# Optimization experiments

Measured on AMD Instinct MI355X. Metric: run time of the kernel, lower is better.

## Reference

```python
import jax, jax.numpy as jnp
import numpy as np

B, S, D, E = 32, 16, 64, 768  # batch, max summary segments, max doc splits, embed dim
EPS = 1e-12


def _l2norm(x):
    # tf.nn.l2_normalize: x * rsqrt(max(sum(x^2), eps))
    return x * jax.lax.rsqrt(jnp.maximum(jnp.sum(x * x, axis=-1, keepdims=True), EPS))


def setup_inputs() -> dict:
    key = jax.random.key(0)
    ks = jax.random.split(key, 12)
    nd = jax.random.randint(ks[0], (B,), 1, D + 1)
    ns = jax.random.randint(ks[1], (B,), 1, S + 1)
    doc = jax.random.normal(ks[2], (B, D, E), jnp.float32)
    seg = jax.random.normal(ks[3], (B, S, E), jnp.float32)
    # emulate RaggedTensor.to_tensor(): zero padding beyond ragged lengths
    doc = doc * (jnp.arange(D)[None, :, None] < nd[:, None, None])
    seg = seg * (jnp.arange(S)[None, :, None] < ns[:, None, None])
    tis = jax.random.uniform(ks[4], (B, S), jnp.float32)
    tis = jnp.where(jnp.arange(S)[None, :] < ns[:, None], tis, 1.0)
    tagg = jax.random.uniform(ks[5], (B,), jnp.float32)
    s1, s2, s3 = 1.0 / np.sqrt(2 * E), 1.0 / np.sqrt(E), 1.0 / np.sqrt(E // 2)
    W1 = jax.random.normal(ks[6], (2 * E, E), jnp.float32) * s1
    W2 = jax.random.normal(ks[7], (E, E // 2), jnp.float32) * s2
    W3 = jax.random.normal(ks[8], (E // 2, 1), jnp.float32) * s3
    return {
        'document_splits_embedding': doc,
        'summary_sentences_embedding': seg,
        'num_document_splits': nd,
        'num_summary_segments': ns,
        'target_agg_score': tagg,
        'target_instance_score': tis,
        'W1': W1, 'b1': jnp.zeros((E,), jnp.float32),
        'W2': W2, 'b2': jnp.zeros((E // 2,), jnp.float32),
        'W3': W3, 'b3': jnp.zeros((1,), jnp.float32),
    }


def reference(document_splits_embedding, summary_sentences_embedding,
              num_document_splits, num_summary_segments,
              target_agg_score, target_instance_score,
              W1, b1, W2, b2, W3, b3):
    doc, seg = document_splits_embedding, summary_sentences_embedding
    nd, ns = num_document_splits, num_summary_segments
    b, d, e = doc.shape
    s = seg.shape[1]
    nsf = ns.astype(jnp.float32)

    # target_instance_score padded with 1.0 beyond ragged length (done in setup; pass through)
    tis = target_instance_score

    # ---- pairwise MLP over all (segment, doc_split) pairs ----
    pair = jnp.concatenate([
        jnp.broadcast_to(doc[:, None, :, :], (b, s, d, e)),
        jnp.broadcast_to(seg[:, :, None, :], (b, s, d, e)),
    ], axis=-1)                                             # [B,S,D,2E]
    h = jax.nn.gelu(pair @ W1 + b1, approximate=False)      # [B,S,D,E]
    h = jax.nn.gelu(h @ W2 + b2, approximate=False)         # [B,S,D,E/2]
    mlp_out = jax.nn.sigmoid(h @ W3 + b3)[..., 0]           # [B,S,D]

    doc_mask = (jnp.arange(d)[None, :] < nd[:, None]).astype(jnp.float32)  # [B,D]
    scored = doc_mask[:, None, :] * mlp_out                # mask invalid doc splits
    pred0 = jnp.max(scored, axis=2)                         # [B,S]
    seg_scale = jnp.where(ns > 10, 1.0, 100.0)[:, None]     # faithful to mask+(1-mask)*100
    pred = seg_scale * pred0                                # [B,S]

    # ---- cosine similarity prior (keras CosineSimilarity = -cos) ----
    dn = _l2norm(doc)                                       # [B,D,E]
    sn = _l2norm(seg)                                       # [B,S,E]
    cos = jnp.einsum('bse,bde->bsd', sn, dn)                # [B,S,D]
    sim = doc_mask[:, None, :] * (1.0 + (-cos)) / 2.0
    doc_cos = jnp.max(sim, axis=2)                          # [B,S]
    seg_mask = (jnp.arange(s)[None, :] < ns[:, None]).astype(jnp.float32)
    diff = jnp.abs(doc_cos - pred) * seg_mask
    cos_prior = jnp.mean(jnp.sum(diff, axis=1) / nsf)

    # ---- correlation prior: Pearson correlation over the 768 'sample' axis ----
    c = seg - jnp.mean(seg, axis=-1, keepdims=True)
    z = c * jax.lax.rsqrt(jnp.maximum(jnp.sum(c * c, axis=-1, keepdims=True), EPS))
    R = (1.0 + jnp.einsum('bse,bte->bst', z, z)) / 2.0      # [B,S,S]
    p = pred
    t1 = (1.0 - p)[:, :, None] * (1.0 - p)[:, None, :]
    t2 = p[:, :, None] * p[:, None, :]
    pair_mask = seg_mask[:, :, None] * seg_mask[:, None, :]
    term = jnp.abs(t1 - R) * jnp.abs(t2 - R) * pair_mask
    corr_prior = jnp.mean(jnp.sum(term, axis=(1, 2)) / nsf)

    return (target_agg_score, tis, pred, ns, cos_prior, corr_prior)
```

## Files before the change

### kernel.cpp

```cpp
#include <hip/hip_runtime.h>
#include <hip/hip_bf16.h>
#include <math.h>

#define EPSF 1e-12f

typedef short bf16x8 __attribute__((ext_vector_type(8)));
typedef float f32x4  __attribute__((ext_vector_type(4)));

__device__ __forceinline__ float gelu_fast(float x) {
    float x2 = x * x;
    float z = -2.3021184f * x * fmaf(0.044715f, x2, 1.0f);
    float u = __builtin_amdgcn_exp2f(z);
    return x * __builtin_amdgcn_rcpf(1.0f + u);
}
__device__ __forceinline__ float sigmoid_fast(float x) {
    float u = __builtin_amdgcn_exp2f(-1.44269504f * x);
    return __builtin_amdgcn_rcpf(1.0f + u);
}
__device__ __forceinline__ float bf2f(unsigned short u) {
    return __uint_as_float(((unsigned int)u) << 16);
}
__device__ __forceinline__ unsigned short f2bf(float f) {
    unsigned int u = __float_as_uint(f);
    u += 0x7FFFu + ((u >> 16) & 1u);
    return (unsigned short)(u >> 16);
}

__global__ __launch_bounds__(256) void k_prep(
    const float* __restrict__ doc, const float* __restrict__ seg,
    const float* __restrict__ W1, const float* __restrict__ W2,
    const float* __restrict__ tagg, const float* __restrict__ tis,
    const int* __restrict__ ns,
    float* __restrict__ dscale, float* __restrict__ sscale,
    float* __restrict__ smean, float* __restrict__ cscale,
    unsigned short* __restrict__ docB, unsigned short* __restrict__ segB,
    unsigned short* __restrict__ W1T, unsigned short* __restrict__ W2T,
    float* __restrict__ out)
{
    __shared__ float sT[64][65];
    int blk = blockIdx.x;
    int t = threadIdx.x;
    if (blk == 1000) {
        if (t < 32) out[t] = tagg[t];
        out[32 + t] = tis[t];
        out[32 + 256 + t] = tis[256 + t];
        if (t < 32) out[1056 + t] = (float)ns[t];
        return;
    }
    if (blk < 640) {
        int row = blk * 4 + (t >> 6);
        int lane = t & 63;
        const float* src = (row < 2048) ? (doc + (size_t)row * 768)
                                        : (seg + (size_t)(row - 2048) * 768);
        unsigned short* dst = (row < 2048) ? (docB + (size_t)row * 768)
                                           : (segB + (size_t)(row - 2048) * 768);
        float ss = 0.f, sm = 0.f;
        float4 v0 = *(const float4*)(src + lane * 4);
        float4 v1 = *(const float4*)(src + lane * 4 + 256);
        float4 v2 = *(const float4*)(src + lane * 4 + 512);
        ss += v0.x * v0.x + v0.y * v0.y + v0.z * v0.z + v0.w * v0.w;
        ss += v1.x * v1.x + v1.y * v1.y + v1.z * v1.z + v1.w * v1.w;
        ss += v2.x * v2.x + v2.y * v2.y + v2.z * v2.z + v2.w * v2.w;
        sm += v0.x + v0.y + v0.z + v0.w;
        sm += v1.x + v1.y + v1.z + v1.w;
        sm += v2.x + v2.y + v2.z + v2.w;
        {
            ushort4 o;
            o.x = f2bf(v0.x); o.y = f2bf(v0.y); o.z = f2bf(v0.z); o.w = f2bf(v0.w);
            *(ushort4*)(dst + lane * 4) = o;
            o.x = f2bf(v1.x); o.y = f2bf(v1.y); o.z = f2bf(v1.z); o.w = f2bf(v1.w);
            *(ushort4*)(dst + lane * 4 + 256) = o;
            o.x = f2bf(v2.x); o.y = f2bf(v2.y); o.z = f2bf(v2.z); o.w = f2bf(v2.w);
            *(ushort4*)(dst + lane * 4 + 512) = o;
        }
        #pragma unroll
        for (int off = 32; off > 0; off >>= 1) {
            ss += __shfl_down(ss, off);
            sm += __shfl_down(sm, off);
        }
        if (lane == 0) {
            if (row < 2048) {
                dscale[row] = rsqrtf(fmaxf(ss, EPSF));
            } else {
                int r = row - 2048;
                sscale[r] = rsqrtf(fmaxf(ss, EPSF));
                float mean = sm * (1.0f / 768.0f);
                smean[r] = mean;
                cscale[r] = rsqrtf(fmaxf(ss - sm * mean, EPSF));
            }
        }
        return;
    }
    int tt = blk - 640;
    const float* in; unsigned short* out2; int R, C, bx, by;
    if (tt < 288) { in = W1; out2 = W1T; R = 1536; C = 768; bx = tt % 12; by = tt / 12; }
    else { tt -= 288; in = W2; out2 = W2T; R = 768; C = 384; bx = tt % 6; by = tt / 6; }
    int c0 = bx * 64, r0 = by * 64;
    int tr = t >> 2, tc4 = (t & 3) * 16;
    #pragma unroll
    for (int i = 0; i < 4; ++i) {
        float4 v = *(const float4*)(in + (size_t)(r0 + tr) * C + c0 + tc4 + i * 4);
        sT[tr][tc4 + i * 4 + 0] = v.x; sT[tr][tc4 + i * 4 + 1] = v.y;
        sT[tr][tc4 + i * 4 + 2] = v.z; sT[tr][tc4 + i * 4 + 3] = v.w;
    }
    __syncthreads();
    union { uint4 v; unsigned short u[8]; } o0, o1;
    #pragma unroll
    for (int i = 0; i < 8; ++i) o0.u[i] = f2bf(sT[tc4 + i][tr]);
    #pragma unroll
    for (int i = 0; i < 8; ++i) o1.u[i] = f2bf(sT[tc4 + 8 + i][tr]);
    *(uint4*)(out2 + (size_t)(c0 + tr) * R + r0 + tc4) = o0.v;
    *(uint4*)(out2 + (size_t)(c0 + tr) * R + r0 + tc4 + 8) = o1.v;
}

__global__ __launch_bounds__(256) void k_l1(
    const unsigned short* __restrict__ docB, const unsigned short* __restrict__ segB,
    const unsigned short* __restrict__ W1T_bf, const float* __restrict__ b1,
    unsigned short* __restrict__ XdocB, unsigned short* __restrict__ XsegB)
{
    int mb = blockIdx.x;
    int n0 = blockIdx.y * 128;
    int t = threadIdx.x, w = t >> 6, l = t & 63;
    int lm = l & 15, kh = l >> 4;
    bool isdoc = (mb < 32);
    int m0 = isdoc ? mb * 64 : (mb - 32) * 64;
    const unsigned short* A = isdoc ? docB : segB;
    int koff = isdoc ? 0 : 768;
    unsigned short* C = isdoc ? XdocB : XsegB;

    const unsigned short* gA = A + (size_t)(m0 + lm) * 768 + kh * 8;
    const unsigned short* gB = W1T_bf + (size_t)(n0 + w * 32 + lm) * 1536 + koff + kh * 8;

    f32x4 acc[4][2];
    #pragma unroll
    for (int mt = 0; mt < 4; ++mt)
        #pragma unroll
        for (int nt = 0; nt < 2; ++nt) acc[mt][nt] = (f32x4){0.f, 0.f, 0.f, 0.f};

    bf16x8 a0A[4], a1A[4], b0A[2], b1A[2];
    bf16x8 a0B[4], a1B[4], b0B[2], b1B[2];
    #pragma unroll
    for (int mt = 0; mt < 4; ++mt) {
        a0A[mt] = *(const bf16x8*)(gA + (size_t)mt * 16 * 768);
        a1A[mt] = *(const bf16x8*)(gA + (size_t)mt * 16 * 768 + 32);
    }
    #pragma unroll
    for (int nt = 0; nt < 2; ++nt) {
        b0A[nt] = *(const bf16x8*)(gB + (size_t)nt * 16 * 1536);
        b1A[nt] = *(const bf16x8*)(gB + (size_t)nt * 16 * 1536 + 32);
    }

    #define L1_BODY(KT, A0, A1, B0, B1, NA0, NA1, NB0, NB1)                     \
    {                                                                           \
        if ((KT) < 11) {                                                        \
            int ko = ((KT) + 1) * 64;                                           \
            _Pragma("unroll")                                                   \
            for (int mt = 0; mt < 4; ++mt) {                                    \
                NA0[mt] = *(const bf16x8*)(gA + (size_t)mt * 16 * 768 + ko);    \
                NA1[mt] = *(const bf16x8*)(gA + (size_t)mt * 16 * 768 + ko + 32); \
            }                                                                   \
            _Pragma("unroll")                                                   \
            for (int nt = 0; nt < 2; ++nt) {                                    \
                NB0[nt] = *(const bf16x8*)(gB + (size_t)nt * 16 * 1536 + ko);   \
                NB1[nt] = *(const bf16x8*)(gB + (size_t)nt * 16 * 1536 + ko + 32); \
            }                                                                   \
        }                                                                       \
        _Pragma("unroll")                                                       \
        for (int mt = 0; mt < 4; ++mt)                                          \
            _Pragma("unroll")                                                   \
            for (int nt = 0; nt < 2; ++nt)                                      \
                acc[mt][nt] = __builtin_amdgcn_mfma_f32_16x16x32_bf16(          \
                    A0[mt], B0[nt], acc[mt][nt], 0, 0, 0);                      \
        _Pragma("unroll")                                                       \
        for (int mt = 0; mt < 4; ++mt)                                          \
            _Pragma("unroll")                                                   \
            for (int nt = 0; nt < 2; ++nt)                                      \
                acc[mt][nt] = __builtin_amdgcn_mfma_f32_16x16x32_bf16(          \
                    A1[mt], B1[nt], acc[mt][nt], 0, 0, 0);                      \
    }

    for (int kt2 = 0; kt2 < 12; kt2 += 2) {
        L1_BODY(kt2,     a0A, a1A, b0A, b1A, a0B, a1B, b0B, b1B);
        L1_BODY(kt2 + 1, a0B, a1B, b0B, b1B, a0A, a1A, b0A, b1A);
    }
    #undef L1_BODY

    #pragma unroll
    for (int nt = 0; nt < 2; ++nt) {
        int n = n0 + w * 32 + nt * 16 + lm;
        float bv = isdoc ? 0.f : b1[n];
        #pragma unroll
        for (int mt = 0; mt < 4; ++mt)
            #pragma unroll
            for (int j = 0; j < 4; ++j) {
                int row = m0 + mt * 16 + kh * 4 + j;
                C[(size_t)row * 768 + n] = f2bf(acc[mt][nt][j] + bv);
            }
    }
}

__global__ __launch_bounds__(256, 2) void k_fused_mfma(
    const unsigned short* __restrict__ XdocB, const unsigned short* __restrict__ XsegB,
    const unsigned short* __restrict__ W2T_bf,
    const float* __restrict__ b2, const float* __restrict__ W3, const float* __restrict__ b3,
    const int* __restrict__ nd, const int* __restrict__ ns,
    const unsigned short* __restrict__ docB, const unsigned short* __restrict__ segB,
    const float* __restrict__ seg,
    const float* __restrict__ dscale, const float* __restrict__ sscale,
    const float* __restrict__ smean, const float* __restrict__ cscale,
    float* __restrict__ out_pred, float* __restrict__ predv,
    float* __restrict__ dcws, float* __restrict__ Rws)
{
    __shared__ union {
        struct {
            unsigned short sA0[64 * 64];
            unsigned short sA1[64 * 64];
            float sXseg[768];
            float sRed[64][4];
        } p;
        struct { float sRedC[16][4]; } c;
        struct { unsigned short zb[16][776]; } r;
    } U;

    int blk = blockIdx.x;
    int t = threadIdx.x, w = t >> 6, l = t & 63;
    int lm = l & 15, kh = l >> 4;

    if (blk >= 512) {
        if (blk < 544) {
            int b = blk - 512;
            const unsigned short* gS = segB + (size_t)(b * 16 + lm) * 768 + kh * 8;
            const unsigned short* gD = docB + (size_t)(b * 64 + w * 16 + lm) * 768 + kh * 8;
            f32x4 acc = (f32x4){0.f, 0.f, 0.f, 0.f};
            for (int kt = 0; kt < 24; ++kt) {
                bf16x8 a = *(const bf16x8*)(gS + kt * 32);
                bf16x8 bb = *(const bf16x8*)(gD + kt * 32);
                acc = __builtin_amdgcn_mfma_f32_16x16x32_bf16(a, bb, acc, 0, 0, 0);
            }
            int ndb = nd[b];
            int d = w * 16 + lm;
            float dsc = dscale[b * 64 + d];
            #pragma unroll
            for (int j = 0; j < 4; ++j) {
                int s = kh * 4 + j;
                float cosv = acc[j] * sscale[b * 16 + s] * dsc;
                float sim = (d < ndb) ? (1.0f - cosv) * 0.5f : 0.f;
                sim = fmaxf(sim, __shfl_xor(sim, 1));
                sim = fmaxf(sim, __shfl_xor(sim, 2));
                sim = fmaxf(sim, __shfl_xor(sim, 4));
                sim = fmaxf(sim, __shfl_xor(sim, 8));
                if (lm == 0) U.c.sRedC[s][w] = sim;
            }
            __syncthreads();
            if (t < 16) {
                float dc = fmaxf(fmaxf(U.c.sRedC[t][0], U.c.sRedC[t][1]),
                                 fmaxf(U.c.sRedC[t][2], U.c.sRedC[t][3]));
                dcws[b * 16 + t] = dc;
            }
        } else {
            int b = blk - 544;
            for (int i = t; i < 16 * 768; i += 256) {
                int s = i / 768; int e = i - s * 768;
                U.r.zb[s][e] = f2bf((seg[((size_t)b * 16 + s) * 768 + e]
                                     - smean[b * 16 + s]) * cscale[b * 16 + s]);
            }
            __syncthreads();
            if (w == 0) {
                f32x4 acc = (f32x4){0.f, 0.f, 0.f, 0.f};
                #pragma unroll
                for (int kt = 0; kt < 24; ++kt) {
                    bf16x8 z = *(const bf16x8*)&U.r.zb[lm][kt * 32 + kh * 8];
                    acc = __builtin_amdgcn_mfma_f32_16x16x32_bf16(z, z, acc, 0, 0, 0);
                }
                #pragma unroll
                for (int j = 0; j < 4; ++j) {
                    int row = kh * 4 + j;
                    Rws[b * 256 + row * 16 + lm] = 0.5f * (1.0f + acc[j]);
                }
            }
        }
        return;
    }

    int bs = blk;
    int b = bs >> 4;
    int sw2 = (lm & 7) << 4;

    for (int i = t; i < 768; i += 256) U.p.sXseg[i] = bf2f(XsegB[(size_t)bs * 768 + i]);

    const int ndb = nd[b];
    const float segscale = (ns[b] > 10) ? 1.0f : 100.0f;
    const float b3v = b3[0];

    f32x4 acc[4][6];
    #pragma unroll
    for (int mt = 0; mt < 4; ++mt)
        #pragma unroll
        for (int nt = 0; nt < 6; ++nt) acc[mt][nt] = (f32x4){0.f, 0.f, 0.f, 0.f};

    int ar = t >> 2, ak = (t & 3) * 16;
    int asw = (ar & 7) << 4;
    const char* gXd = (const char*)XdocB + (size_t)(b * 64 + ar) * 1536;
    const unsigned short* gW2w = W2T_bf + (size_t)(w * 96 + lm) * 768 + kh * 8;

    union u128 { uint4 v; unsigned short u[8]; };

    bf16x8 bbA[6], bbB[6];
    #pragma unroll
    for (int nt = 0; nt < 6; ++nt)
        bbA[nt] = *(const bf16x8*)(gW2w + (size_t)nt * 16 * 768);

    {
        u128 xc0, xc1;
        xc0.v = *(const uint4*)(gXd + ak * 2);
        xc1.v = *(const uint4*)(gXd + ak * 2 + 16);
        __syncthreads();
        u128 o0, o1;
        #pragma unroll
        for (int i = 0; i < 8; ++i)
            o0.u[i] = f2bf(gelu_fast(bf2f(xc0.u[i]) + U.p.sXseg[ak + i]));
        #pragma unroll
        for (int i = 0; i < 8; ++i)
            o1.u[i] = f2bf(gelu_fast(bf2f(xc1.u[i]) + U.p.sXseg[ak + 8 + i]));
        *(uint4*)((char*)U.p.sA0 + ar * 128 + ((ak * 2) ^ asw)) = o0.v;
        *(uint4*)((char*)U.p.sA0 + ar * 128 + ((ak * 2 + 16) ^ asw)) = o1.v;
    }

    #pragma unroll
    for (int kt = 0; kt < 12; ++kt) {
        unsigned short* cbuf = (kt & 1) ? U.p.sA1 : U.p.sA0;
        unsigned short* nbuf = (kt & 1) ? U.p.sA0 : U.p.sA1;
        __syncthreads();
        u128 xn0, xn1;
        if (kt < 11) {
            xn0.v = *(const uint4*)(gXd + (kt + 1) * 128 + ak * 2);
            xn1.v = *(const uint4*)(gXd + (kt + 1) * 128 + ak * 2 + 16);
        }
        {
            #pragma unroll
            for (int nt = 0; nt < 6; ++nt)
                bbB[nt] = *(const bf16x8*)(gW2w + (size_t)nt * 16 * 768 + kt * 64 + 32);
            int kb = (kh * 16) ^ sw2;
            bf16x8 a[4];
            #pragma unroll
            for (int mt = 0; mt < 4; ++mt)
                a[mt] = *(const bf16x8*)((const char*)cbuf + (mt * 16 + lm) * 128 + kb);
            __builtin_amdgcn_s_setprio(1);
            #pragma unroll
            for (int mt = 0; mt < 4; ++mt)
                #pragma unroll
                for (int nt = 0; nt < 6; ++nt)
                    acc[mt][nt] = __builtin_amdgcn_mfma_f32_16x16x32_bf16(
                        a[mt], bbA[nt], acc[mt][nt], 0, 0, 0);
            __builtin_amdgcn_s_setprio(0);
        }
        {
            if (kt < 11) {
                #pragma unroll
                for (int nt = 0; nt < 6; ++nt)
                    bbA[nt] = *(const bf16x8*)(gW2w + (size_t)nt * 16 * 768 + (kt + 1) * 64);
            }
            int kb = (64 + kh * 16) ^ sw2;
            bf16x8 a[4];
            #pragma unroll
            for (int mt = 0; mt < 4; ++mt)
                a[mt] = *(const bf16x8*)((const char*)cbuf + (mt * 16 + lm) * 128 + kb);
            __builtin_amdgcn_s_setprio(1);
            #pragma unroll
            for (int mt = 0; mt < 4; ++mt)
                #pragma unroll
                for (int nt = 0; nt < 6; ++nt)
                    acc[mt][nt] = __builtin_amdgcn_mfma_f32_16x16x32_bf16(
                        a[mt], bbB[nt], acc[mt][nt], 0, 0, 0);
            __builtin_amdgcn_s_setprio(0);
        }
        if (kt < 11) {
            u128 o0, o1;
            #pragma unroll
            for (int i = 0; i < 8; ++i)
                o0.u[i] = f2bf(gelu_fast(bf2f(xn0.u[i]) + U.p.sXseg[(kt + 1) * 64 + ak + i]));
            #pragma unroll
            for (int i = 0; i < 8; ++i)
                o1.u[i] = f2bf(gelu_fast(bf2f(xn1.u[i]) + U.p.sXseg[(kt + 1) * 64 + ak + 8 + i]));
            *(uint4*)((char*)nbuf + ar * 128 + ((ak * 2) ^ asw)) = o0.v;
            *(uint4*)((char*)nbuf + ar * 128 + ((ak * 2 + 16) ^ asw)) = o1.v;
        }
    }

    float b2v[6], w3v[6];
    #pragma unroll
    for (int nt = 0; nt < 6; ++nt) {
        int n = w * 96 + nt * 16 + lm;
        b2v[nt] = b2[n]; w3v[nt] = W3[n];
    }
    #pragma unroll
    for (int mt = 0; mt < 4; ++mt) {
        #pragma unroll
        for (int j = 0; j < 4; ++j) {
            float s = 0.f;
            #pragma unroll
            for (int nt = 0; nt < 6; ++nt)
                s += gelu_fast(acc[mt][nt][j] + b2v[nt]) * w3v[nt];
            s += __shfl_xor(s, 1); s += __shfl_xor(s, 2);
            s += __shfl_xor(s, 4); s += __shfl_xor(s, 8);
            if (lm == 0) U.p.sRed[mt * 16 + kh * 4 + j][w] = s;
        }
    }
    __syncthreads();
    if (w == 0) {
        float h3 = U.p.sRed[l][0] + U.p.sRed[l][1] + U.p.sRed[l][2] + U.p.sRed[l][3] + b3v;
        float sig = sigmoid_fast(h3);
        float val = (l < ndb) ? sig : 0.f;
        #pragma unroll
        for (int off = 32; off > 0; off >>= 1) val = fmaxf(val, __shfl_xor(val, off));
        if (l == 0) {
            float pv = segscale * val;
            out_pred[bs] = pv;
            predv[bs] = pv;
        }
    }
}

__global__ __launch_bounds__(256) void k_final(
    const int* __restrict__ ns, const float* __restrict__ dcws,
    const float* __restrict__ Rws, const float* __restrict__ predv,
    float* __restrict__ out)
{
    __shared__ float sl1[32], sl2[32];
    int t = threadIdx.x;
    if (t < 32) {
        int nsb = ns[t];
        float sb = 0.f;
        #pragma unroll
        for (int s = 0; s < 16; ++s) {
            float d = fabsf(dcws[t * 16 + s] - predv[t * 16 + s]);
            sb += (s < nsb) ? d : 0.f;
        }
        sl1[t] = sb / (float)nsb;
    }
    {
        int b = t >> 3, c = t & 7;
        int nsb = ns[b];
        float sum = 0.f;
        #pragma unroll
        for (int k = 0; k < 32; ++k) {
            int idx = c * 32 + k;
            int s = idx >> 4, tt = idx & 15;
            float R = Rws[b * 256 + idx];
            float ps = predv[b * 16 + s], pt = predv[b * 16 + tt];
            float t1 = (1.f - ps) * (1.f - pt), t2 = ps * pt;
            float term = fabsf(t1 - R) * fabsf(t2 - R);
            sum += (s < nsb && tt < nsb) ? term : 0.f;
        }
        sum += __shfl_xor(sum, 1);
        sum += __shfl_xor(sum, 2);
        sum += __shfl_xor(sum, 4);
        if (c == 0) sl2[b] = sum / (float)nsb;
    }
    __syncthreads();
    if (t == 0) {
        float a = 0.f, bsum = 0.f;
        #pragma unroll
        for (int i = 0; i < 32; ++i) { a += sl1[i]; bsum += sl2[i]; }
        out[1088] = a * (1.0f / 32.0f);
        out[1089] = bsum * (1.0f / 32.0f);
    }
}

extern "C" void kernel_launch(void* const* d_in, const int* in_sizes, int n_in,
                              void* d_out, int out_size, void* d_ws, size_t ws_size,
                              hipStream_t stream)
{
    const float* doc  = (const float*)d_in[0];
    const float* seg  = (const float*)d_in[1];
    const int*   nd   = (const int*)d_in[2];
    const int*   ns   = (const int*)d_in[3];
    const float* tagg = (const float*)d_in[4];
    const float* tis  = (const float*)d_in[5];
    const float* W1   = (const float*)d_in[6];
    const float* b1   = (const float*)d_in[7];
    const float* W2   = (const float*)d_in[8];
    const float* b2   = (const float*)d_in[9];
    const float* W3   = (const float*)d_in[10];
    const float* b3   = (const float*)d_in[11];
    float* out = (float*)d_out;

    float* fws      = (float*)d_ws;
    float* dscale   = fws;
    float* sscale   = dscale + 2048;
    float* smean    = sscale + 512;
    float* cscale   = smean + 512;
    float* predv    = cscale + 512;
    float* dcws     = predv + 512;
    float* Rws      = dcws + 512;
    unsigned short* docB  = (unsigned short*)(Rws + 8192);
    unsigned short* segB  = docB + (size_t)2048 * 768;
    unsigned short* W1T   = segB + (size_t)512 * 768;
    unsigned short* W2T   = W1T + (size_t)768 * 1536;
    unsigned short* XdocB = W2T + (size_t)384 * 768;
    unsigned short* XsegB = XdocB + (size_t)2048 * 768;

    k_prep<<<1001, 256, 0, stream>>>(doc, seg, W1, W2, tagg, tis, ns,
                                     dscale, sscale, smean, cscale,
                                     docB, segB, W1T, W2T, out);
    k_l1<<<dim3(40, 6), 256, 0, stream>>>(docB, segB, W1T, b1, XdocB, XsegB);
    k_fused_mfma<<<576, 256, 0, stream>>>(XdocB, XsegB, W2T, b2, W3, b3, nd, ns,
                                          docB, segB, seg, dscale, sscale,
                                          smean, cscale, out + 544, predv,
                                          dcws, Rws);
    k_final<<<1, 256, 0, stream>>>(ns, dcws, Rws, predv, out);
}
```

Baseline: 82.58 us.

## Fuse final reduction into main kernel via last-block atomic and recompute norms locally

Removes the separate k_final launch by having the last finishing block of k_fused_mfma, found through an atomic done-counter, perform the final loss reductions. Row norms and means are no longer computed in k_prep; the cosine blocks compute them from bf16 data inside their MFMA loop, and the correlation blocks compute them from fp32 seg. The main MLP blocks are also remapped so neighbouring blocks span different batches. This saves one kernel launch and some workspace traffic, at the cost of extra ALU work in the small blocks and a norm computed from bf16-rounded values.

```diff
diff --git a/kernel.cpp b/kernel.cpp
--- a/kernel.cpp
+++ b/kernel.cpp
@@ -31,22 +31,13 @@
     const float* __restrict__ W1, const float* __restrict__ W2,
     const float* __restrict__ tagg, const float* __restrict__ tis,
     const int* __restrict__ ns,
-    float* __restrict__ dscale, float* __restrict__ sscale,
-    float* __restrict__ smean, float* __restrict__ cscale,
     unsigned short* __restrict__ docB, unsigned short* __restrict__ segB,
     unsigned short* __restrict__ W1T, unsigned short* __restrict__ W2T,
-    float* __restrict__ out)
+    float* __restrict__ out, unsigned int* __restrict__ donecnt)
 {
     __shared__ float sT[64][65];
     int blk = blockIdx.x;
     int t = threadIdx.x;
-    if (blk == 1000) {
-        if (t < 32) out[t] = tagg[t];
-        out[32 + t] = tis[t];
-        out[32 + 256 + t] = tis[256 + t];
-        if (t < 32) out[1056 + t] = (float)ns[t];
-        return;
-    }
     if (blk < 640) {
         int row = blk * 4 + (t >> 6);
         int lane = t & 63;
@@ -54,41 +45,24 @@
                                         : (seg + (size_t)(row - 2048) * 768);
         unsigned short* dst = (row < 2048) ? (docB + (size_t)row * 768)
                                            : (segB + (size_t)(row - 2048) * 768);
-        float ss = 0.f, sm = 0.f;
         float4 v0 = *(const float4*)(src + lane * 4);
         float4 v1 = *(const float4*)(src + lane * 4 + 256);
         float4 v2 = *(const float4*)(src + lane * 4 + 512);
-        ss += v0.x * v0.x + v0.y * v0.y + v0.z * v0.z + v0.w * v0.w;
-        ss += v1.x * v1.x + v1.y * v1.y + v1.z * v1.z + v1.w * v1.w;
-        ss += v2.x * v2.x + v2.y * v2.y + v2.z * v2.z + v2.w * v2.w;
-        sm += v0.x + v0.y + v0.z + v0.w;
-        sm += v1.x + v1.y + v1.z + v1.w;
-        sm += v2.x + v2.y + v2.z + v2.w;
-        {
-            ushort4 o;
-            o.x = f2bf(v0.x); o.y = f2bf(v0.y); o.z = f2bf(v0.z); o.w = f2bf(v0.w);
-            *(ushort4*)(dst + lane * 4) = o;
-            o.x = f2bf(v1.x); o.y = f2bf(v1.y); o.z = f2bf(v1.z); o.w = f2bf(v1.w);
-            *(ushort4*)(dst + lane * 4 + 256) = o;
-            o.x = f2bf(v2.x); o.y = f2bf(v2.y); o.z = f2bf(v2.z); o.w = f2bf(v2.w);
-            *(ushort4*)(dst + lane * 4 + 512) = o;
-        }
-        #pragma unroll
-        for (int off = 32; off > 0; off >>= 1) {
-            ss += __shfl_down(ss, off);
-            sm += __shfl_down(sm, off);
-        }
-        if (lane == 0) {
-            if (row < 2048) {
-                dscale[row] = rsqrtf(fmaxf(ss, EPSF));
-            } else {
-                int r = row - 2048;
-                sscale[r] = rsqrtf(fmaxf(ss, EPSF));
-                float mean = sm * (1.0f / 768.0f);
-                smean[r] = mean;
-                cscale[r] = rsqrtf(fmaxf(ss - sm * mean, EPSF));
-            }
-        }
+        ushort4 o;
+        o.x = f2bf(v0.x); o.y = f2bf(v0.y); o.z = f2bf(v0.z); o.w = f2bf(v0.w);
+        *(ushort4*)(dst + lane * 4) = o;
+        o.x = f2bf(v1.x); o.y = f2bf(v1.y); o.z = f2bf(v1.z); o.w = f2bf(v1.w);
+        *(ushort4*)(dst + lane * 4 + 256) = o;
+        o.x = f2bf(v2.x); o.y = f2bf(v2.y); o.z = f2bf(v2.z); o.w = f2bf(v2.w);
+        *(ushort4*)(dst + lane * 4 + 512) = o;
+        return;
+    }
+    if (blk == 1000) {
+        if (t == 0) *donecnt = 0u;
+        if (t < 32) out[t] = tagg[t];
+        out[32 + t] = tis[t];
+        out[32 + 256 + t] = tis[256 + t];
+        if (t < 32) out[1056 + t] = (float)ns[t];
         return;
     }
     int tt = blk - 640;
@@ -206,10 +180,9 @@
     const int* __restrict__ nd, const int* __restrict__ ns,
     const unsigned short* __restrict__ docB, const unsigned short* __restrict__ segB,
     const float* __restrict__ seg,
-    const float* __restrict__ dscale, const float* __restrict__ sscale,
-    const float* __restrict__ smean, const float* __restrict__ cscale,
     float* __restrict__ out_pred, float* __restrict__ predv,
-    float* __restrict__ dcws, float* __restrict__ Rws)
+    float* __restrict__ dcws, float* __restrict__ Rws,
+    unsigned int* __restrict__ donecnt, float* __restrict__ out)
 {
     __shared__ union {
         struct {
@@ -218,13 +191,16 @@
             float sXseg[768];
             float sRed[64][4];
         } p;
-        struct { float sRedC[16][4]; } c;
-        struct { unsigned short zb[16][776]; } r;
+        struct { float sS16[16]; float sRedC[16][4]; } c;
+        struct { unsigned short zb[16][776]; float smL[16]; float csL[16]; } r;
+        struct { float sl1[32]; float sl2[32]; } f;
     } U;
+    __shared__ int isLast;
 
     int blk = blockIdx.x;
     int t = threadIdx.x, w = t >> 6, l = t & 63;
     int lm = l & 15, kh = l >> 4;
+    union u128 { uint4 v; unsigned short u[8]; };
 
     if (blk >= 512) {
         if (blk < 544) {
@@ -232,18 +208,30 @@
             const unsigned short* gS = segB + (size_t)(b * 16 + lm) * 768 + kh * 8;
             const unsigned short* gD = docB + (size_t)(b * 64 + w * 16 + lm) * 768 + kh * 8;
             f32x4 acc = (f32x4){0.f, 0.f, 0.f, 0.f};
+            float ssS = 0.f, ssD = 0.f;
             for (int kt = 0; kt < 24; ++kt) {
                 bf16x8 a = *(const bf16x8*)(gS + kt * 32);
                 bf16x8 bb = *(const bf16x8*)(gD + kt * 32);
+                #pragma unroll
+                for (int j = 0; j < 8; ++j) {
+                    float sv = bf2f((unsigned short)a[j]);
+                    float dv = bf2f((unsigned short)bb[j]);
+                    ssS = fmaf(sv, sv, ssS);
+                    ssD = fmaf(dv, dv, ssD);
+                }
                 acc = __builtin_amdgcn_mfma_f32_16x16x32_bf16(a, bb, acc, 0, 0, 0);
             }
+            ssS += __shfl_xor(ssS, 16); ssS += __shfl_xor(ssS, 32);
+            ssD += __shfl_xor(ssD, 16); ssD += __shfl_xor(ssD, 32);
+            float dscale_own = rsqrtf(fmaxf(ssD, EPSF));
+            if (w == 0 && kh == 0) U.c.sS16[lm] = rsqrtf(fmaxf(ssS, EPSF));
+            __syncthreads();
             int ndb = nd[b];
             int d = w * 16 + lm;
-            float dsc = dscale[b * 64 + d];
             #pragma unroll
             for (int j = 0; j < 4; ++j) {
                 int s = kh * 4 + j;
-                float cosv = acc[j] * sscale[b * 16 + s] * dsc;
+                float cosv = acc[j] * U.c.sS16[s] * dscale_own;
                 float sim = (d < ndb) ? (1.0f - cosv) * 0.5f : 0.f;
                 sim = fmaxf(sim, __shfl_xor(sim, 1));
                 sim = fmaxf(sim, __shfl_xor(sim, 2));
@@ -259,10 +247,32 @@
             }
         } else {
             int b = blk - 544;
+            #pragma unroll
+            for (int j = 0; j < 4; ++j) {
+                int r = w * 4 + j;
+                const float* src = seg + (size_t)(b * 16 + r) * 768;
+                float ss = 0.f, sm = 0.f;
+                #pragma unroll
+                for (int i = 0; i < 12; ++i) {
+                    float x = src[l + 64 * i];
+                    ss += x * x; sm += x;
+                }
+                #pragma unroll
+                for (int off = 32; off > 0; off >>= 1) {
+                    ss += __shfl_down(ss, off);
+                    sm += __shfl_down(sm, off);
+                }
+                if (l == 0) {
+                    float mean = sm * (1.0f / 768.0f);
+                    U.r.smL[r] = mean;
+                    U.r.csL[r] = rsqrtf(fmaxf(ss - sm * mean, EPSF));
+                }
+            }
+            __syncthreads();
             for (int i = t; i < 16 * 768; i += 256) {
                 int s = i / 768; int e = i - s * 768;
                 U.r.zb[s][e] = f2bf((seg[((size_t)b * 16 + s) * 768 + e]
-                                     - smean[b * 16 + s]) * cscale[b * 16 + s]);
+                                     - U.r.smL[s]) * U.r.csL[s]);
             }
             __syncthreads();
             if (w == 0) {
@@ -279,155 +289,155 @@
                 }
             }
         }
-        return;
-    }
-
-    int bs = blk;
-    int b = bs >> 4;
-    int sw2 = (lm & 7) << 4;
-
-    for (int i = t; i < 768; i += 256) U.p.sXseg[i] = bf2f(XsegB[(size_t)bs * 768 + i]);
-
-    const int ndb = nd[b];
-    const float segscale = (ns[b] > 10) ? 1.0f : 100.0f;
-    const float b3v = b3[0];
-
-    f32x4 acc[4][6];
-    #pragma unroll
-    for (int mt = 0; mt < 4; ++mt)
-        #pragma unroll
-        for (int nt = 0; nt < 6; ++nt) acc[mt][nt] = (f32x4){0.f, 0.f, 0.f, 0.f};
-
-    int ar = t >> 2, ak = (t & 3) * 16;
-    int asw = (ar & 7) << 4;
-    const char* gXd = (const char*)XdocB + (size_t)(b * 64 + ar) * 1536;
-    const unsigned short* gW2w = W2T_bf + (size_t)(w * 96 + lm) * 768 + kh * 8;
-
-    union u128 { uint4 v; unsigned short u[8]; };
-
-    bf16x8 bbA[6], bbB[6];
-    #pragma unroll
-    for (int nt = 0; nt < 6; ++nt)
-        bbA[nt] = *(const bf16x8*)(gW2w + (size_t)nt * 16 * 768);
-
-    {
-        u128 xc0, xc1;
-        xc0.v = *(const uint4*)(gXd + ak * 2);
-        xc1.v = *(const uint4*)(gXd + ak * 2 + 16);
+    } else {
+        int p = blk;
+        int bs = (p & 7) * 64 + (p >> 3);
+        int b = bs >> 4;
+        int sw2 = (lm & 7) << 4;
+
+        for (int i = t; i < 768; i += 256) U.p.sXseg[i] = bf2f(XsegB[(size_t)bs * 768 + i]);
+
+        const int ndb = nd[b];
+        const float segscale = (ns[b] > 10) ? 1.0f : 100.0f;
+        const float b3v = b3[0];
+
+        f32x4 acc[4][6];
+        #pragma unroll
+        for (int mt = 0; mt < 4; ++mt)
+            #pragma unroll
+            for (int nt = 0; nt < 6; ++nt) acc[mt][nt] = (f32x4){0.f, 0.f, 0.f, 0.f};
+
+        int ar = t >> 2, ak = (t & 3) * 16;
+        int asw = (ar & 7) << 4;
+        const char* gXd = (const char*)XdocB + (size_t)(b * 64 + ar) * 1536;
+        const unsigned short* gW2w = W2T_bf + (size_t)(w * 96 + lm) * 768 + kh * 8;
+
+        bf16x8 bbA[6], bbB[6];
+        #pragma unroll
+        for (int nt = 0; nt < 6; ++nt)
+            bbA[nt] = *(const bf16x8*)(gW2w + (size_t)nt * 16 * 768);
+
+        {
+            u128 xc0, xc1;
+            xc0.v = *(const uint4*)(gXd + ak * 2);
+            xc1.v = *(const uint4*)(gXd + ak * 2 + 16);
+            __syncthreads();
+            u128 o0, o1;
+            #pragma unroll
+            for (int i = 0; i < 8; ++i)
+                o0.u[i] = f2bf(gelu_fast(bf2f(xc0.u[i]) + U.p.sXseg[ak + i]));
+            #pragma unroll
+            for (int i = 0; i < 8; ++i)
+                o1.u[i] = f2bf(gelu_fast(bf2f(xc1.u[i]) + U.p.sXseg[ak + 8 + i]));
+            *(uint4*)((char*)U.p.sA0 + ar * 128 + ((ak * 2) ^ asw)) = o0.v;
+            *(uint4*)((char*)U.p.sA0 + ar * 128 + ((ak * 2 + 16) ^ asw)) = o1.v;
+        }
+
+        #pragma unroll
+        for (int kt = 0; kt < 12; ++kt) {
+            unsigned short* cbuf = (kt & 1) ? U.p.sA1 : U.p.sA0;
+            unsigned short* nbuf = (kt & 1) ? U.p.sA0 : U.p.sA1;
+            __syncthreads();
+            u128 xn0, xn1;
+            if (kt < 11) {
+                xn0.v = *(const uint4*)(gXd + (kt + 1) * 128 + ak * 2);
+                xn1.v = *(const uint4*)(gXd + (kt + 1) * 128 + ak * 2 + 16);
+            }
+            {
+                #pragma unroll
+                for (int nt = 0; nt < 6; ++nt)
+                    bbB[nt] = *(const bf16x8*)(gW2w + (size_t)nt * 16 * 768 + kt * 64 + 32);
+                int kb = (kh * 16) ^ sw2;
+                bf16x8 a[4];
+                #pragma unroll
+                for (int mt = 0; mt < 4; ++mt)
+                    a[mt] = *(const bf16x8*)((const char*)cbuf + (mt * 16 + lm) * 128 + kb);
+                __builtin_amdgcn_s_setprio(1);
+                #pragma unroll
+                for (int mt = 0; mt < 4; ++mt)
+                    #pragma unroll
+                    for (int nt = 0; nt < 6; ++nt)
+                        acc[mt][nt] = __builtin_amdgcn_mfma_f32_16x16x32_bf16(
+                            a[mt], bbA[nt], acc[mt][nt], 0, 0, 0);
+                __builtin_amdgcn_s_setprio(0);
+            }
+            {
+                if (kt < 11) {
+                    #pragma unroll
+                    for (int nt = 0; nt < 6; ++nt)
+                        bbA[nt] = *(const bf16x8*)(gW2w + (size_t)nt * 16 * 768 + (kt + 1) * 64);
+                }
+                int kb = (64 + kh * 16) ^ sw2;
+                bf16x8 a[4];
+                #pragma unroll
+                for (int mt = 0; mt < 4; ++mt)
+                    a[mt] = *(const bf16x8*)((const char*)cbuf + (mt * 16 + lm) * 128 + kb);
+                __builtin_amdgcn_s_setprio(1);
+                #pragma unroll
+                for (int mt = 0; mt < 4; ++mt)
+                    #pragma unroll
+                    for (int nt = 0; nt < 6; ++nt)
+                        acc[mt][nt] = __builtin_amdgcn_mfma_f32_16x16x32_bf16(
+                            a[mt], bbB[nt], acc[mt][nt], 0, 0, 0);
+                __builtin_amdgcn_s_setprio(0);
+            }
+            if (kt < 11) {
+                u128 o0, o1;
+                #pragma unroll
+                for (int i = 0; i < 8; ++i)
+                    o0.u[i] = f2bf(gelu_fast(bf2f(xn0.u[i]) + U.p.sXseg[(kt + 1) * 64 + ak + i]));
+                #pragma unroll
+                for (int i = 0; i < 8; ++i)
+                    o1.u[i] = f2bf(gelu_fast(bf2f(xn1.u[i]) + U.p.sXseg[(kt + 1) * 64 + ak + 8 + i]));
+                *(uint4*)((char*)nbuf + ar * 128 + ((ak * 2) ^ asw)) = o0.v;
+                *(uint4*)((char*)nbuf + ar * 128 + ((ak * 2 + 16) ^ asw)) = o1.v;
+            }
+        }
+
+        float b2v[6], w3v[6];
+        #pragma unroll
+        for (int nt = 0; nt < 6; ++nt) {
+            int n = w * 96 + nt * 16 + lm;
+            b2v[nt] = b2[n]; w3v[nt] = W3[n];
+        }
+        #pragma unroll
+        for (int mt = 0; mt < 4; ++mt) {
+            #pragma unroll
+            for (int j = 0; j < 4; ++j) {
+                float s = 0.f;
+                #pragma unroll
+                for (int nt = 0; nt < 6; ++nt)
+                    s += gelu_fast(acc[mt][nt][j] + b2v[nt]) * w3v[nt];
+                s += __shfl_xor(s, 1); s += __shfl_xor(s, 2);
+                s += __shfl_xor(s, 4); s += __shfl_xor(s, 8);
+                if (lm == 0) U.p.sRed[mt * 16 + kh * 4 + j][w] = s;
+            }
+        }
         __syncthreads();
-        u128 o0, o1;
-        #pragma unroll
-        for (int i = 0; i < 8; ++i)
-            o0.u[i] = f2bf(gelu_fast(bf2f(xc0.u[i]) + U.p.sXseg[ak + i]));
-        #pragma unroll
-        for (int i = 0; i < 8; ++i)
-            o1.u[i] = f2bf(gelu_fast(bf2f(xc1.u[i]) + U.p.sXseg[ak + 8 + i]));
-        *(uint4*)((char*)U.p.sA0 + ar * 128 + ((ak * 2) ^ asw)) = o0.v;
-        *(uint4*)((char*)U.p.sA0 + ar * 128 + ((ak * 2 + 16) ^ asw)) = o1.v;
-    }
-
-    #pragma unroll
-    for (int kt = 0; kt < 12; ++kt) {
-        unsigned short* cbuf = (kt & 1) ? U.p.sA1 : U.p.sA0;
-        unsigned short* nbuf = (kt & 1) ? U.p.sA0 : U.p.sA1;
-        __syncthreads();
-        u128 xn0, xn1;
-        if (kt < 11) {
-            xn0.v = *(const uint4*)(gXd + (kt + 1) * 128 + ak * 2);
-            xn1.v = *(const uint4*)(gXd + (kt + 1) * 128 + ak * 2 + 16);
-        }
-        {
-            #pragma unroll
-            for (int nt = 0; nt < 6; ++nt)
-                bbB[nt] = *(const bf16x8*)(gW2w + (size_t)nt * 16 * 768 + kt * 64 + 32);
-            int kb = (kh * 16) ^ sw2;
-            bf16x8 a[4];
-            #pragma unroll
-            for (int mt = 0; mt < 4; ++mt)
-                a[mt] = *(const bf16x8*)((const char*)cbuf + (mt * 16 + lm) * 128 + kb);
-            __builtin_amdgcn_s_setprio(1);
-            #pragma unroll
-            for (int mt = 0; mt < 4; ++mt)
-                #pragma unroll
-                for (int nt = 0; nt < 6; ++nt)
-                    acc[mt][nt] = __builtin_amdgcn_mfma_f32_16x16x32_bf16(
-                        a[mt], bbA[nt], acc[mt][nt], 0, 0, 0);
-            __builtin_amdgcn_s_setprio(0);
-        }
-        {
-            if (kt < 11) {
-                #pragma unroll
-                for (int nt = 0; nt < 6; ++nt)
-                    bbA[nt] = *(const bf16x8*)(gW2w + (size_t)nt * 16 * 768 + (kt + 1) * 64);
-            }
-            int kb = (64 + kh * 16) ^ sw2;
-            bf16x8 a[4];
-            #pragma unroll
-            for (int mt = 0; mt < 4; ++mt)
-                a[mt] = *(const bf16x8*)((const char*)cbuf + (mt * 16 + lm) * 128 + kb);
-            __builtin_amdgcn_s_setprio(1);
-            #pragma unroll
-            for (int mt = 0; mt < 4; ++mt)
-                #pragma unroll
-                for (int nt = 0; nt < 6; ++nt)
-                    acc[mt][nt] = __builtin_amdgcn_mfma_f32_16x16x32_bf16(
-                        a[mt], bbB[nt], acc[mt][nt], 0, 0, 0);
-            __builtin_amdgcn_s_setprio(0);
-        }
-        if (kt < 11) {
-            u128 o0, o1;
-            #pragma unroll
-            for (int i = 0; i < 8; ++i)
-                o0.u[i] = f2bf(gelu_fast(bf2f(xn0.u[i]) + U.p.sXseg[(kt + 1) * 64 + ak + i]));
-            #pragma unroll
-            for (int i = 0; i < 8; ++i)
-                o1.u[i] = f2bf(gelu_fast(bf2f(xn1.u[i]) + U.p.sXseg[(kt + 1) * 64 + ak + 8 + i]));
-            *(uint4*)((char*)nbuf + ar * 128 + ((ak * 2) ^ asw)) = o0.v;
-            *(uint4*)((char*)nbuf + ar * 128 + ((ak * 2 + 16) ^ asw)) = o1.v;
-        }
-    }
-
-    float b2v[6], w3v[6];
-    #pragma unroll
-    for (int nt = 0; nt < 6; ++nt) {
-        int n = w * 96 + nt * 16 + lm;
-        b2v[nt] = b2[n]; w3v[nt] = W3[n];
-    }
-    #pragma unroll
-    for (int mt = 0; mt < 4; ++mt) {
-        #pragma unroll
-        for (int j = 0; j < 4; ++j) {
-            float s = 0.f;
-            #pragma unroll
-            for (int nt = 0; nt < 6; ++nt)
-                s += gelu_fast(acc[mt][nt][j] + b2v[nt]) * w3v[nt];
-            s += __shfl_xor(s, 1); s += __shfl_xor(s, 2);
-            s += __shfl_xor(s, 4); s += __shfl_xor(s, 8);
-            if (lm == 0) U.p.sRed[mt * 16 + kh * 4 + j][w] = s;
-        }
-    }
+        if (w == 0) {
+            float h3 = U.p.sRed[l][0] + U.p.sRed[l][1] + U.p.sRed[l][2] + U.p.sRed[l][3] + b3v;
+            float sig = sigmoid_fast(h3);
+            float val = (l < ndb) ? sig : 0.f;
+            #pragma unroll
+            for (int off = 32; off > 0; off >>= 1) val = fmaxf(val, __shfl_xor(val, off));
+            if (l == 0) {
+                float pv = segscale * val;
+                out_pred[bs] = pv;
+                predv[bs] = pv;
+            }
+        }
+    }
+
     __syncthreads();
-    if (w == 0) {
-        float h3 = U.p.sRed[l][0] + U.p.sRed[l][1] + U.p.sRed[l][2] + U.p.sRed[l][3] + b3v;
-        float sig = sigmoid_fast(h3);
-        float val = (l < ndb) ? sig : 0.f;
-        #pragma unroll
-        for (int off = 32; off > 0; off >>= 1) val = fmaxf(val, __shfl_xor(val, off));
-        if (l == 0) {
-            float pv = segscale * val;
-            out_pred[bs] = pv;
-            predv[bs] = pv;
-        }
-    }
-}
-
-__global__ __launch_bounds__(256) void k_final(
-    const int* __restrict__ ns, const float* __restrict__ dcws,
-    const float* __restrict__ Rws, const float* __restrict__ predv,
-    float* __restrict__ out)
-{
-    __shared__ float sl1[32], sl2[32];
-    int t = threadIdx.x;
+    if (t == 0) {
+        __threadfence();
+        unsigned int old = atomicAdd(donecnt, 1u);
+        isLast = (old == 575u);
+    }
+    __syncthreads();
+    if (!isLast) return;
+    __threadfence();
+
     if (t < 32) {
         int nsb = ns[t];
         float sb = 0.f;
@@ -436,7 +446,7 @@
             float d = fabsf(dcws[t * 16 + s] - predv[t * 16 + s]);
             sb += (s < nsb) ? d : 0.f;
         }
-        sl1[t] = sb / (float)nsb;
+        U.f.sl1[t] = sb / (float)nsb;
     }
     {
         int b = t >> 3, c = t & 7;
@@ -445,23 +455,23 @@
         #pragma unroll
         for (int k = 0; k < 32; ++k) {
             int idx = c * 32 + k;
-            int s = idx >> 4, tt = idx & 15;
+            int s = idx >> 4, tt2 = idx & 15;
             float R = Rws[b * 256 + idx];
-            float ps = predv[b * 16 + s], pt = predv[b * 16 + tt];
+            float ps = predv[b * 16 + s], pt = predv[b * 16 + tt2];
             float t1 = (1.f - ps) * (1.f - pt), t2 = ps * pt;
             float term = fabsf(t1 - R) * fabsf(t2 - R);
-            sum += (s < nsb && tt < nsb) ? term : 0.f;
+            sum += (s < nsb && tt2 < nsb) ? term : 0.f;
         }
         sum += __shfl_xor(sum, 1);
         sum += __shfl_xor(sum, 2);
         sum += __shfl_xor(sum, 4);
-        if (c == 0) sl2[b] = sum / (float)nsb;
+        if (c == 0) U.f.sl2[b] = sum / (float)nsb;
     }
     __syncthreads();
     if (t == 0) {
         float a = 0.f, bsum = 0.f;
         #pragma unroll
-        for (int i = 0; i < 32; ++i) { a += sl1[i]; bsum += sl2[i]; }
+        for (int i = 0; i < 32; ++i) { a += U.f.sl1[i]; bsum += U.f.sl2[i]; }
         out[1088] = a * (1.0f / 32.0f);
         out[1089] = bsum * (1.0f / 32.0f);
     }
@@ -485,15 +495,12 @@
     const float* b3   = (const float*)d_in[11];
     float* out = (float*)d_out;
 
-    float* fws      = (float*)d_ws;
-    float* dscale   = fws;
-    float* sscale   = dscale + 2048;
-    float* smean    = sscale + 512;
-    float* cscale   = smean + 512;
-    float* predv    = cscale + 512;
-    float* dcws     = predv + 512;
-    float* Rws      = dcws + 512;
-    unsigned short* docB  = (unsigned short*)(Rws + 8192);
+    float* fws   = (float*)d_ws;
+    float* predv = fws;
+    float* dcws  = predv + 512;
+    float* Rws   = dcws + 512;
+    unsigned int* donecnt = (unsigned int*)(Rws + 8192);
+    unsigned short* docB  = (unsigned short*)(donecnt + 16);
     unsigned short* segB  = docB + (size_t)2048 * 768;
     unsigned short* W1T   = segB + (size_t)512 * 768;
     unsigned short* W2T   = W1T + (size_t)768 * 1536;
@@ -501,12 +508,9 @@
     unsigned short* XsegB = XdocB + (size_t)2048 * 768;
 
     k_prep<<<1001, 256, 0, stream>>>(doc, seg, W1, W2, tagg, tis, ns,
-                                     dscale, sscale, smean, cscale,
-                                     docB, segB, W1T, W2T, out);
+                                     docB, segB, W1T, W2T, out, donecnt);
     k_l1<<<dim3(40, 6), 256, 0, stream>>>(docB, segB, W1T, b1, XdocB, XsegB);
     k_fused_mfma<<<576, 256, 0, stream>>>(XdocB, XsegB, W2T, b2, W3, b3, nd, ns,
-                                          docB, segB, seg, dscale, sscale,
-                                          smean, cscale, out + 544, predv,
-                                          dcws, Rws);
-    k_final<<<1, 256, 0, stream>>>(ns, dcws, Rws, predv, out);
-}
+                                          docB, segB, seg, out + 544, predv,
+                                          dcws, Rws, donecnt, out);
+}
```

Result: slower. 96.17 us (+16.5%).
